# Optimization experiments

Hardware: AMD Instinct MI355X
Metric: run time of the kernel (lower is better)

The kernel has to match this reference:

```python
import jax, jax.numpy as jnp
import numpy as np

BS, DEG, H = 32, 4, 32
OUT = H  # n_aggr=1 inside Full -> out_size = n_aggr * h_size = h_size


def setup_inputs() -> dict:
    key = jax.random.key(0)
    k1, k2 = jax.random.split(key)
    neighbour_h = jax.random.normal(k1, (BS, DEG, H), dtype=jnp.float32)
    hp1 = H + 1
    t_shape = (hp1,) * DEG + (OUT,)  # [33,33,33,33,32]
    # xavier_uniform-like scale: fan_in = hp1**DEG, fan_out = OUT
    scale = float(np.sqrt(2.0 / (hp1 ** DEG + OUT)))
    T = jax.random.normal(k2, t_shape, dtype=jnp.float32) * scale
    return {"neighbour_h": neighbour_h, "T": T}


def reference(neighbour_h, T):
    # Full.forward: chunk neighbour_h along child dim, feed to AugmentedTensor.
    # AugmentedTensor: sequentially contract T against each child's augmented
    # embedding [h_i ; 1] over the leading axes of T.
    bs, deg, h = neighbour_h.shape
    hp1 = h + 1
    # augment with trailing 1 (bias slot): [bs, deg, h+1]
    h_aug = jnp.concatenate(
        [neighbour_h, jnp.ones((bs, deg, 1), neighbour_h.dtype)], axis=2
    )
    # first contraction: [bs, hp1] @ [hp1, hp1^(deg-1)*out]
    res = jnp.matmul(h_aug[:, 0, :], T.reshape(hp1, -1))
    # remaining contractions shrink the trailing dim by hp1 each step
    for i in range(1, deg):
        res = jnp.einsum("bi,bio->bo", h_aug[:, i, :], res.reshape(bs, hp1, -1))
    return res  # [bs, out_size] == [bs, h_size] since n_aggr=1
```

## Files before the change

### kernel.cpp

```cpp
#include <hip/hip_runtime.h>
#include <hip/hip_bf16.h>

#define HSZ 32
#define HP1 33
#define M3 35937
#define TI_STRIDE 1149984
#define TIB ((size_t)TI_STRIDE * 4)
#define NBLK 1124
#define NT 64
#define DEPTH 6
#define NHT 6144
#define NHTG_FLOATS 4352

#define OFF_TILES 32768

typedef short bf16x8 __attribute__((ext_vector_type(8)));
typedef float f32x16 __attribute__((ext_vector_type(16)));

__device__ inline short f2bf(float f) {
  __hip_bfloat16 h = __float2bfloat16(f);
  return __builtin_bit_cast(short, h);
}

__global__ __launch_bounds__(256) void k_pre(const float* __restrict__ nh,
                                             float* __restrict__ nhTg,
                                             float* __restrict__ tiles) {
  const int blk = (int)blockIdx.x;
  const int t = (int)threadIdx.x;
  if (blk < 64) {
    ((float4*)tiles)[blk * 256 + t] = make_float4(0.f, 0.f, 0.f, 0.f);
  } else {
    for (int x = t; x < NHTG_FLOATS; x += 256) {
      float v = 0.f;
      if (x < 4224) {
        const int d = x / 1056;
        const int rem = x - d * 1056;
        const int row = rem >> 5;
        const int b = rem & 31;
        v = (row < HSZ) ? nh[b * 128 + d * 32 + row] : 1.0f;
      }
      nhTg[x] = v;
    }
  }
}

__global__ __launch_bounds__(64) void k_main(const float* __restrict__ T,
                                             const float* __restrict__ nhTg,
                                             float* __restrict__ tiles) {
  __shared__ float lds[DEPTH * 1024 + NHTG_FLOATS];
  const int blk = blockIdx.x;
  const int m0 = blk * 32;
  const int l = (int)threadIdx.x;
  const int bo = l & 31;
  const int g = l >> 5;

  const int mrel = l >> 3;
  size_t src[4];
#pragma unroll
  for (int q = 0; q < 4; ++q) {
    const bool valid = (m0 + 8 * q + mrel) < M3;
    src[q] = valid ? ((size_t)(m0 * 32 + q * 256 + l * 4) * 4) : 0;
  }
  const char* Tb = (const char*)T;
  const char* Ng = (const char*)nhTg;

#pragma unroll
  for (int q = 0; q < 17; ++q) {
    __builtin_amdgcn_global_load_lds(
        (const __attribute__((address_space(1))) void*)(Ng + q * 1024 + l * 16),
        (__attribute__((address_space(3))) void*)(&lds[NHT + q * 256]),
        16, 0, 0);
  }

#define ISSUE(row_, slot_)                                                    \
  {                                                                           \
    _Pragma("unroll")                                                         \
    for (int q = 0; q < 4; ++q) {                                             \
      __builtin_amdgcn_global_load_lds(                                       \
          (const __attribute__((address_space(1))) void*)(                    \
              Tb + (size_t)(row_)*TIB + src[q]),                              \
          (__attribute__((address_space(3))) void*)(                          \
              &lds[(slot_)*1024 + q * 256]),                                  \
          16, 0, 0);                                                          \
    }                                                                         \
  }

  ISSUE(0, 0) ISSUE(1, 1) ISSUE(2, 2) ISSUE(3, 3) ISSUE(4, 4) ISSUE(5, 5)

  asm volatile("s_waitcnt vmcnt(24)" ::: "memory");
  __builtin_amdgcn_sched_barrier(0);

  float df0[8], df1[8];
#pragma unroll
  for (int e = 0; e < 8; ++e) {
#pragma unroll
    for (int half = 0; half < 2; ++half) {
      const int m = m0 + 16 * half + 8 * g + e;
      const bool valid = m < M3;
      const int mc = valid ? m : (M3 - 1);
      const int j = mc / 1089;
      const int r = mc - j * 1089;
      const int kk = r / 33;
      const int ll = r - kk * 33;
      const float a1 = lds[NHT + 1056 + j * 32 + bo];
      const float a2 = lds[NHT + 2112 + kk * 32 + bo];
      const float a3 = lds[NHT + 3168 + ll * 32 + bo];
      const float v = valid ? (a1 * a2 * a3) : 0.0f;
      if (half == 0) df0[e] = v; else df1[e] = v;
    }
  }

  f32x16 acc = {};

#define STEP(i_, vm_, doIssue_)                                               \
  {                                                                           \
    asm volatile("s_waitcnt vmcnt(" #vm_ ")" ::: "memory");                   \
    __builtin_amdgcn_sched_barrier(0);                                        \
    float tv0[8], tv1[8];                                                     \
    const float a0 = lds[NHT + (i_)*32 + bo];                                 \
    _Pragma("unroll")                                                         \
    for (int e = 0; e < 8; ++e) {                                             \
      tv0[e] = lds[((i_) % DEPTH) * 1024 + (8 * g + e) * 32 + bo];            \
      tv1[e] = lds[((i_) % DEPTH) * 1024 + 512 + (8 * g + e) * 32 + bo];      \
    }                                                                         \
    bf16x8 af0, bf0, af1, bf1;                                                \
    _Pragma("unroll")                                                         \
    for (int e = 0; e < 8; ++e) {                                             \
      af0[e] = f2bf(a0 * df0[e]);                                             \
      bf0[e] = f2bf(tv0[e]);                                                  \
      af1[e] = f2bf(a0 * df1[e]);                                             \
      bf1[e] = f2bf(tv1[e]);                                                  \
    }                                                                         \
    acc = __builtin_amdgcn_mfma_f32_32x32x16_bf16(af0, bf0, acc, 0, 0, 0);    \
    acc = __builtin_amdgcn_mfma_f32_32x32x16_bf16(af1, bf1, acc, 0, 0, 0);    \
    if (doIssue_) {                                                           \
      asm volatile("s_waitcnt lgkmcnt(0)" ::: "memory");                      \
      __builtin_amdgcn_sched_barrier(0);                                      \
      ISSUE((i_) + DEPTH, (i_) % DEPTH)                                       \
    }                                                                         \
  }

  STEP(0, 20, 1)  STEP(1, 20, 1)  STEP(2, 20, 1)  STEP(3, 20, 1)
  STEP(4, 20, 1)  STEP(5, 20, 1)  STEP(6, 20, 1)  STEP(7, 20, 1)
  STEP(8, 20, 1)  STEP(9, 20, 1)  STEP(10, 20, 1) STEP(11, 20, 1)
  STEP(12, 20, 1) STEP(13, 20, 1) STEP(14, 20, 1) STEP(15, 20, 1)
  STEP(16, 20, 1) STEP(17, 20, 1) STEP(18, 20, 1) STEP(19, 20, 1)
  STEP(20, 20, 1) STEP(21, 20, 1) STEP(22, 20, 1) STEP(23, 20, 1)
  STEP(24, 20, 1) STEP(25, 20, 1) STEP(26, 20, 1) STEP(27, 20, 0)
  STEP(28, 16, 0) STEP(29, 12, 0) STEP(30, 8, 0)  STEP(31, 4, 0)
  STEP(32, 0, 0)
#undef STEP
#undef ISSUE

  float* tp = tiles + (size_t)(blk & (NT - 1)) * 1024;
#pragma unroll
  for (int r = 0; r < 16; ++r) {
    const int brow = (r & 3) + 8 * (r >> 2) + 4 * g;
    atomicAdd(tp + brow * 32 + bo, acc[r]);
  }
}

__global__ __launch_bounds__(256) void k_red(const float* __restrict__ tiles,
                                             float* __restrict__ out) {
  const int idx = blockIdx.x * 256 + (int)threadIdx.x;
  float s = 0.f;
  for (int t = 0; t < NT; ++t) s += tiles[(size_t)t * 1024 + idx];
  out[idx] = s;
}

extern "C" void kernel_launch(void* const* d_in, const int* in_sizes, int n_in,
                              void* d_out, int out_size, void* d_ws, size_t ws_size,
                              hipStream_t stream) {
  const float* nh = (const float*)d_in[0];
  const float* T  = (const float*)d_in[1];
  float* out = (float*)d_out;
  char* ws = (char*)d_ws;
  float* nhTg  = (float*)ws;
  float* tiles = (float*)(ws + OFF_TILES);

  k_pre<<<65, 256, 0, stream>>>(nh, nhTg, tiles);
  k_main<<<NBLK, 64, 0, stream>>>(T, nhTg, tiles);
  k_red<<<4, 256, 0, stream>>>(tiles, out);
}
```

Measured before the change: 39.28 us.

## Partition work by (i,j) slabs with precomputed outer-product D23 streamed from global

The main kernel is repartitioned so each block owns one (i,j) pair and streams a contiguous 1089x32 span of T, instead of a 32-row slice across all 33 leading indices. The product of the third and fourth child embeddings is precomputed once into a global D23 table and streamed into LDS alongside T. The per-block scalar c = h0[i]*h1[j] is applied to that table before one MFMA per step, replacing the per-block divisions and the doubled MFMA per row. In exchange the kernel reads the D23 table from global memory (likely L2-resident), runs 69 steps per block instead of 33, and handles the odd tail row with a special load.

```diff
diff --git a/kernel.cpp b/kernel.cpp
--- a/kernel.cpp
+++ b/kernel.cpp
@@ -2,17 +2,14 @@
 #include <hip/hip_bf16.h>
 
 #define HSZ 32
-#define HP1 33
-#define M3 35937
-#define TI_STRIDE 1149984
-#define TIB ((size_t)TI_STRIDE * 4)
-#define NBLK 1124
+#define KL 1089
+#define KLP 1104
+#define NBLK 1089
 #define NT 64
 #define DEPTH 6
-#define NHT 6144
-#define NHTG_FLOATS 4352
 
-#define OFF_TILES 32768
+#define OFF_D23   16384
+#define OFF_TILES 163840
 
 typedef short bf16x8 __attribute__((ext_vector_type(8)));
 typedef float f32x16 __attribute__((ext_vector_type(16)));
@@ -24,132 +21,147 @@
 
 __global__ __launch_bounds__(256) void k_pre(const float* __restrict__ nh,
                                              float* __restrict__ nhTg,
+                                             float* __restrict__ D23T,
                                              float* __restrict__ tiles) {
   const int blk = (int)blockIdx.x;
   const int t = (int)threadIdx.x;
   if (blk < 64) {
     ((float4*)tiles)[blk * 256 + t] = make_float4(0.f, 0.f, 0.f, 0.f);
+  } else if (blk < 70) {
+    for (int x = (blk - 64) * 256 + t; x < KLP * 32; x += 6 * 256) {
+      const int kl = x >> 5;
+      const int b = x & 31;
+      float v = 0.f;
+      if (kl < KL) {
+        const int k = kl / 33;
+        const int l = kl - k * 33;
+        const float a2 = (k < HSZ) ? nh[b * 128 + 64 + k] : 1.0f;
+        const float a3 = (l < HSZ) ? nh[b * 128 + 96 + l] : 1.0f;
+        v = a2 * a3;
+      }
+      D23T[x] = v;
+    }
   } else {
-    for (int x = t; x < NHTG_FLOATS; x += 256) {
-      float v = 0.f;
-      if (x < 4224) {
-        const int d = x / 1056;
-        const int rem = x - d * 1056;
-        const int row = rem >> 5;
-        const int b = rem & 31;
-        v = (row < HSZ) ? nh[b * 128 + d * 32 + row] : 1.0f;
-      }
-      nhTg[x] = v;
+    for (int x = t; x < 2 * 1056; x += 256) {
+      const int d = x / 1056;
+      const int rem = x - d * 1056;
+      const int row = rem >> 5;
+      const int b = rem & 31;
+      nhTg[x] = (row < HSZ) ? nh[b * 128 + d * 32 + row] : 1.0f;
     }
   }
 }
 
 __global__ __launch_bounds__(64) void k_main(const float* __restrict__ T,
                                              const float* __restrict__ nhTg,
+                                             const float* __restrict__ D23T,
                                              float* __restrict__ tiles) {
-  __shared__ float lds[DEPTH * 1024 + NHTG_FLOATS];
+  __shared__ float lds[DEPTH * 1024];
   const int blk = blockIdx.x;
-  const int m0 = blk * 32;
+  const int i = blk / 33;
+  const int j = blk - i * 33;
   const int l = (int)threadIdx.x;
   const int bo = l & 31;
   const int g = l >> 5;
 
-  const int mrel = l >> 3;
-  size_t src[4];
-#pragma unroll
-  for (int q = 0; q < 4; ++q) {
-    const bool valid = (m0 + 8 * q + mrel) < M3;
-    src[q] = valid ? ((size_t)(m0 * 32 + q * 256 + l * 4) * 4) : 0;
-  }
-  const char* Tb = (const char*)T;
-  const char* Ng = (const char*)nhTg;
+  const float c = nhTg[i * 32 + bo] * nhTg[1056 + j * 32 + bo];
+  asm volatile("" :: "v"(c) : "memory");
 
-#pragma unroll
-  for (int q = 0; q < 17; ++q) {
-    __builtin_amdgcn_global_load_lds(
-        (const __attribute__((address_space(1))) void*)(Ng + q * 1024 + l * 16),
-        (__attribute__((address_space(3))) void*)(&lds[NHT + q * 256]),
-        16, 0, 0);
-  }
+  const char* Tspan = (const char*)T + ((size_t)i * 35937 + (size_t)j * KL) * 128;
+  const char* Db = (const char*)D23T;
+  const size_t s68_0 = (l < 8) ? ((size_t)68 * 2048 + l * 16) : 0;
 
 #define ISSUE(row_, slot_)                                                    \
   {                                                                           \
     _Pragma("unroll")                                                         \
-    for (int q = 0; q < 4; ++q) {                                             \
+    for (int q = 0; q < 2; ++q) {                                             \
       __builtin_amdgcn_global_load_lds(                                       \
           (const __attribute__((address_space(1))) void*)(                    \
-              Tb + (size_t)(row_)*TIB + src[q]),                              \
+              Tspan + (size_t)(row_)*2048 + q * 1024 + l * 16),               \
           (__attribute__((address_space(3))) void*)(                          \
               &lds[(slot_)*1024 + q * 256]),                                  \
+          16, 0, 0);                                                          \
+    }                                                                         \
+    _Pragma("unroll")                                                         \
+    for (int q = 0; q < 2; ++q) {                                             \
+      __builtin_amdgcn_global_load_lds(                                       \
+          (const __attribute__((address_space(1))) void*)(                    \
+              Db + (size_t)(row_)*2048 + q * 1024 + l * 16),                  \
+          (__attribute__((address_space(3))) void*)(                          \
+              &lds[(slot_)*1024 + 512 + q * 256]),                            \
+          16, 0, 0);                                                          \
+    }                                                                         \
+  }
+#define ISSUE68(slot_)                                                        \
+  {                                                                           \
+    __builtin_amdgcn_global_load_lds(                                         \
+        (const __attribute__((address_space(1))) void*)(Tspan + s68_0),       \
+        (__attribute__((address_space(3))) void*)(&lds[(slot_)*1024]),        \
+        16, 0, 0);                                                            \
+    __builtin_amdgcn_global_load_lds(                                         \
+        (const __attribute__((address_space(1))) void*)(Tspan),               \
+        (__attribute__((address_space(3))) void*)(&lds[(slot_)*1024 + 256]),  \
+        16, 0, 0);                                                            \
+    _Pragma("unroll")                                                         \
+    for (int q = 0; q < 2; ++q) {                                             \
+      __builtin_amdgcn_global_load_lds(                                       \
+          (const __attribute__((address_space(1))) void*)(                    \
+              Db + (size_t)68 * 2048 + q * 1024 + l * 16),                    \
+          (__attribute__((address_space(3))) void*)(                          \
+              &lds[(slot_)*1024 + 512 + q * 256]),                            \
           16, 0, 0);                                                          \
     }                                                                         \
   }
 
   ISSUE(0, 0) ISSUE(1, 1) ISSUE(2, 2) ISSUE(3, 3) ISSUE(4, 4) ISSUE(5, 5)
 
-  asm volatile("s_waitcnt vmcnt(24)" ::: "memory");
-  __builtin_amdgcn_sched_barrier(0);
-
-  float df0[8], df1[8];
-#pragma unroll
-  for (int e = 0; e < 8; ++e) {
-#pragma unroll
-    for (int half = 0; half < 2; ++half) {
-      const int m = m0 + 16 * half + 8 * g + e;
-      const bool valid = m < M3;
-      const int mc = valid ? m : (M3 - 1);
-      const int j = mc / 1089;
-      const int r = mc - j * 1089;
-      const int kk = r / 33;
-      const int ll = r - kk * 33;
-      const float a1 = lds[NHT + 1056 + j * 32 + bo];
-      const float a2 = lds[NHT + 2112 + kk * 32 + bo];
-      const float a3 = lds[NHT + 3168 + ll * 32 + bo];
-      const float v = valid ? (a1 * a2 * a3) : 0.0f;
-      if (half == 0) df0[e] = v; else df1[e] = v;
-    }
-  }
-
   f32x16 acc = {};
 
-#define STEP(i_, vm_, doIssue_)                                               \
+#define STEP(i_, vm_, doIssue_, do68_)                                        \
   {                                                                           \
     asm volatile("s_waitcnt vmcnt(" #vm_ ")" ::: "memory");                   \
     __builtin_amdgcn_sched_barrier(0);                                        \
-    float tv0[8], tv1[8];                                                     \
-    const float a0 = lds[NHT + (i_)*32 + bo];                                 \
+    float tv[8], dv[8];                                                       \
     _Pragma("unroll")                                                         \
     for (int e = 0; e < 8; ++e) {                                             \
-      tv0[e] = lds[((i_) % DEPTH) * 1024 + (8 * g + e) * 32 + bo];            \
-      tv1[e] = lds[((i_) % DEPTH) * 1024 + 512 + (8 * g + e) * 32 + bo];      \
+      tv[e] = lds[((i_) % DEPTH) * 1024 + (8 * g + e) * 32 + bo];             \
+      dv[e] = lds[((i_) % DEPTH) * 1024 + 512 + (8 * g + e) * 32 + bo];       \
     }                                                                         \
-    bf16x8 af0, bf0, af1, bf1;                                                \
+    bf16x8 af, bfr;                                                           \
     _Pragma("unroll")                                                         \
     for (int e = 0; e < 8; ++e) {                                             \
-      af0[e] = f2bf(a0 * df0[e]);                                             \
-      bf0[e] = f2bf(tv0[e]);                                                  \
-      af1[e] = f2bf(a0 * df1[e]);                                             \
-      bf1[e] = f2bf(tv1[e]);                                                  \
+      af[e] = f2bf(c * dv[e]);                                                \
+      bfr[e] = f2bf(tv[e]);                                                   \
     }                                                                         \
-    acc = __builtin_amdgcn_mfma_f32_32x32x16_bf16(af0, bf0, acc, 0, 0, 0);    \
-    acc = __builtin_amdgcn_mfma_f32_32x32x16_bf16(af1, bf1, acc, 0, 0, 0);    \
+    acc = __builtin_amdgcn_mfma_f32_32x32x16_bf16(af, bfr, acc, 0, 0, 0);     \
     if (doIssue_) {                                                           \
       asm volatile("s_waitcnt lgkmcnt(0)" ::: "memory");                      \
       __builtin_amdgcn_sched_barrier(0);                                      \
-      ISSUE((i_) + DEPTH, (i_) % DEPTH)                                       \
+      if (do68_) { ISSUE68((i_) % DEPTH) }                                    \
+      else { ISSUE((i_) + DEPTH, (i_) % DEPTH) }                              \
     }                                                                         \
   }
 
-  STEP(0, 20, 1)  STEP(1, 20, 1)  STEP(2, 20, 1)  STEP(3, 20, 1)
-  STEP(4, 20, 1)  STEP(5, 20, 1)  STEP(6, 20, 1)  STEP(7, 20, 1)
-  STEP(8, 20, 1)  STEP(9, 20, 1)  STEP(10, 20, 1) STEP(11, 20, 1)
-  STEP(12, 20, 1) STEP(13, 20, 1) STEP(14, 20, 1) STEP(15, 20, 1)
-  STEP(16, 20, 1) STEP(17, 20, 1) STEP(18, 20, 1) STEP(19, 20, 1)
-  STEP(20, 20, 1) STEP(21, 20, 1) STEP(22, 20, 1) STEP(23, 20, 1)
-  STEP(24, 20, 1) STEP(25, 20, 1) STEP(26, 20, 1) STEP(27, 20, 0)
-  STEP(28, 16, 0) STEP(29, 12, 0) STEP(30, 8, 0)  STEP(31, 4, 0)
-  STEP(32, 0, 0)
+  STEP(0, 20, 1, 0)  STEP(1, 20, 1, 0)  STEP(2, 20, 1, 0)  STEP(3, 20, 1, 0)
+  STEP(4, 20, 1, 0)  STEP(5, 20, 1, 0)  STEP(6, 20, 1, 0)  STEP(7, 20, 1, 0)
+  STEP(8, 20, 1, 0)  STEP(9, 20, 1, 0)  STEP(10, 20, 1, 0) STEP(11, 20, 1, 0)
+  STEP(12, 20, 1, 0) STEP(13, 20, 1, 0) STEP(14, 20, 1, 0) STEP(15, 20, 1, 0)
+  STEP(16, 20, 1, 0) STEP(17, 20, 1, 0) STEP(18, 20, 1, 0) STEP(19, 20, 1, 0)
+  STEP(20, 20, 1, 0) STEP(21, 20, 1, 0) STEP(22, 20, 1, 0) STEP(23, 20, 1, 0)
+  STEP(24, 20, 1, 0) STEP(25, 20, 1, 0) STEP(26, 20, 1, 0) STEP(27, 20, 1, 0)
+  STEP(28, 20, 1, 0) STEP(29, 20, 1, 0) STEP(30, 20, 1, 0) STEP(31, 20, 1, 0)
+  STEP(32, 20, 1, 0) STEP(33, 20, 1, 0) STEP(34, 20, 1, 0) STEP(35, 20, 1, 0)
+  STEP(36, 20, 1, 0) STEP(37, 20, 1, 0) STEP(38, 20, 1, 0) STEP(39, 20, 1, 0)
+  STEP(40, 20, 1, 0) STEP(41, 20, 1, 0) STEP(42, 20, 1, 0) STEP(43, 20, 1, 0)
+  STEP(44, 20, 1, 0) STEP(45, 20, 1, 0) STEP(46, 20, 1, 0) STEP(47, 20, 1, 0)
+  STEP(48, 20, 1, 0) STEP(49, 20, 1, 0) STEP(50, 20, 1, 0) STEP(51, 20, 1, 0)
+  STEP(52, 20, 1, 0) STEP(53, 20, 1, 0) STEP(54, 20, 1, 0) STEP(55, 20, 1, 0)
+  STEP(56, 20, 1, 0) STEP(57, 20, 1, 0) STEP(58, 20, 1, 0) STEP(59, 20, 1, 0)
+  STEP(60, 20, 1, 0) STEP(61, 20, 1, 0) STEP(62, 20, 1, 1)
+  STEP(63, 20, 0, 0) STEP(64, 16, 0, 0) STEP(65, 12, 0, 0)
+  STEP(66, 8, 0, 0)  STEP(67, 4, 0, 0)  STEP(68, 0, 0, 0)
 #undef STEP
+#undef ISSUE68
 #undef ISSUE
 
   float* tp = tiles + (size_t)(blk & (NT - 1)) * 1024;
@@ -176,9 +188,10 @@
   float* out = (float*)d_out;
   char* ws = (char*)d_ws;
   float* nhTg  = (float*)ws;
+  float* D23T  = (float*)(ws + OFF_D23);
   float* tiles = (float*)(ws + OFF_TILES);
 
-  k_pre<<<65, 256, 0, stream>>>(nh, nhTg, tiles);
-  k_main<<<NBLK, 64, 0, stream>>>(T, nhTg, tiles);
+  k_pre<<<71, 256, 0, stream>>>(nh, nhTg, D23T, tiles);
+  k_main<<<NBLK, 64, 0, stream>>>(T, nhTg, D23T, tiles);
   k_red<<<4, 256, 0, stream>>>(tiles, out);
 }
```

After: 44.37 us. 1.13x slower.
